# Kernel tuning notes

Measured on AMD Instinct MI355X. Metric: run time of the kernel, lower is better.

The kernel has to match this reference:

```python
import jax, jax.numpy as jnp
import numpy as np

B, IN, H, OUT = 8192, 1024, 1024, 1024


def setup_inputs() -> dict:
    key = jax.random.key(0)
    ks = jax.random.split(key, 17)
    n = jax.random.normal
    return {
        "input": n(ks[0], (B, IN), jnp.float32),
        "hidden_state": n(ks[1], (B, H), jnp.float32),
        "cell_state": n(ks[2], (B, H), jnp.float32),
        "W_f": n(ks[3], (IN, H), jnp.float32),
        "U_f": n(ks[4], (H, H), jnp.float32),
        "b_f": n(ks[5], (H,), jnp.float32),
        "W_i": n(ks[6], (IN, H), jnp.float32),
        "U_i": n(ks[7], (H, H), jnp.float32),
        "b_i": n(ks[8], (H,), jnp.float32),
        "W_c": n(ks[9], (IN, H), jnp.float32),
        "U_c": n(ks[10], (H, H), jnp.float32),
        "b_c": n(ks[11], (H,), jnp.float32),
        "W_o": n(ks[12], (IN, H), jnp.float32),
        "U_o": n(ks[13], (H, H), jnp.float32),
        "b_o": n(ks[14], (H,), jnp.float32),
        "W_h": n(ks[15], (H, OUT), jnp.float32),
        "b_h": n(ks[16], (OUT,), jnp.float32),
    }


def reference(input, hidden_state, cell_state,
              W_f, U_f, b_f, W_i, U_i, b_i,
              W_c, U_c, b_c, W_o, U_o, b_o,
              W_h, b_h):
    # Fuse 8 gate matmuls into two grouped GEMMs via concatenated weights.
    W = jnp.concatenate([W_f, W_i, W_c, W_o], axis=1)  # [IN, 4H]
    U = jnp.concatenate([U_f, U_i, U_c, U_o], axis=1)  # [H, 4H]
    b = jnp.concatenate([b_f, b_i, b_c, b_o], axis=0)  # [4H]
    gates = input @ W + hidden_state @ U + b  # [B, 4H]
    f, i, c, o = jnp.split(gates, 4, axis=1)
    f_gate = jax.nn.sigmoid(f)
    i_gate = jax.nn.sigmoid(i)
    c_tilde = jnp.tanh(c)
    o_gate = jax.nn.sigmoid(o)
    cell_state = f_gate * cell_state + i_gate * c_tilde
    hidden_state = o_gate * jnp.tanh(cell_state)
    logits = hidden_state @ W_h + b_h
    output = jax.nn.log_softmax(logits, axis=1)
    return output, hidden_state, cell_state
```

## Files before the change

### kernel.cpp

```cpp
#include <hip/hip_runtime.h>
#include <hip/hip_bf16.h>
#include <cstdint>


#define B_DIM   8192
#define K1      2048
#define H_DIM   1024

typedef __attribute__((ext_vector_type(8))) _Float16 f16x8;
typedef __attribute__((ext_vector_type(4))) float    f32x4;

__device__ __forceinline__ unsigned short f2h_bits(float x) {
    _Float16 h = (_Float16)x;
    return __builtin_bit_cast(unsigned short, h);
}

__device__ __forceinline__ void gload_lds16(const void* g, void* l) {
    __builtin_amdgcn_global_load_lds(
        (const __attribute__((address_space(1))) void*)g,
        (__attribute__((address_space(3))) void*)l, 16, 0, 0);
}

__device__ __forceinline__ f32x4 mfma16(f16x8 a, f16x8 b, f32x4 c) {
    return __builtin_amdgcn_mfma_f32_16x16x32_f16(a, b, c, 0, 0, 0);
}

__device__ __forceinline__ float vexp2(float x) {
    float r; asm("v_exp_f32 %0, %1" : "=v"(r) : "v"(x)); return r;
}
__device__ __forceinline__ float vlog2(float x) {
    float r; asm("v_log_f32 %0, %1" : "=v"(r) : "v"(x)); return r;
}
__device__ __forceinline__ float vrcp(float x) {
    float r; asm("v_rcp_f32 %0, %1" : "=v"(r) : "v"(x)); return r;
}
__device__ __forceinline__ float fast_sigmoid(float v) {
    return vrcp(1.0f + vexp2(-1.44269504f * v));
}
__device__ __forceinline__ float fast_tanh(float v) {
    return 1.0f - 2.0f * vrcp(1.0f + vexp2(2.88539008f * v));
}

__global__ __launch_bounds__(256) void k_split_x(
    const float* __restrict__ input, const float* __restrict__ hidden,
    unsigned short* __restrict__ xhi) {
    const int64_t n4 = (int64_t)B_DIM * K1 / 4;
    for (int64_t i = (int64_t)blockIdx.x * blockDim.x + threadIdx.x; i < n4;
         i += (int64_t)gridDim.x * blockDim.x) {
        int64_t e = i * 4;
        int row = (int)(e >> 11);
        int col = (int)(e & 2047);
        const float* src = (col < 1024) ? (input + (int64_t)row * 1024 + col)
                                        : (hidden + (int64_t)row * 1024 + (col - 1024));
        float4 v = *(const float4*)src;
        ushort4 hv;
        hv.x = f2h_bits(v.x);
        hv.y = f2h_bits(v.y);
        hv.z = f2h_bits(v.z);
        hv.w = f2h_bits(v.w);
        *(ushort4*)(xhi + e) = hv;
    }
}

__global__ __launch_bounds__(256) void k_trans_all(
    const float* __restrict__ W_f, const float* __restrict__ W_i,
    const float* __restrict__ W_c, const float* __restrict__ W_o,
    const float* __restrict__ U_f, const float* __restrict__ U_i,
    const float* __restrict__ U_c, const float* __restrict__ U_o,
    unsigned short* __restrict__ wuhi) {
    const int z = blockIdx.z;
    const float* src;
    if      (z == 0) src = W_f;
    else if (z == 1) src = W_i;
    else if (z == 2) src = W_c;
    else if (z == 3) src = W_o;
    else if (z == 4) src = U_f;
    else if (z == 5) src = U_i;
    else if (z == 6) src = U_c;
    else             src = U_o;
    const int ng = z & 3, koff = (z >> 2) * 1024;

    __shared__ float t[64][65];
    const int h0 = blockIdx.x * 64;
    const int k0 = blockIdx.y * 64;
    const int tx = threadIdx.x & 63, ty = threadIdx.x >> 6;
    #pragma unroll
    for (int r = ty; r < 64; r += 4)
        t[r][tx] = src[(int64_t)(k0 + r) * 1024 + h0 + tx];
    __syncthreads();
    #pragma unroll
    for (int r = ty; r < 64; r += 4) {
        float v = t[tx][r];
        int np = (h0 + r) * 4 + ng;
        wuhi[(int64_t)np * 2048 + koff + k0 + tx] = f2h_bits(v);
    }
}

__global__ __launch_bounds__(256) void k_trans_wh(
    const float* __restrict__ src, unsigned short* __restrict__ whh) {
    __shared__ float t[64][65];
    const int h0 = blockIdx.x * 64;
    const int k0 = blockIdx.y * 64;
    const int tx = threadIdx.x & 63, ty = threadIdx.x >> 6;
    #pragma unroll
    for (int r = ty; r < 64; r += 4)
        t[r][tx] = src[(int64_t)(k0 + r) * 1024 + h0 + tx];
    __syncthreads();
    #pragma unroll
    for (int r = ty; r < 64; r += 4)
        whh[(int64_t)(h0 + r) * 1024 + k0 + tx] = f2h_bits(t[tx][r]);
}

__global__ __launch_bounds__(256) void k_pack_bias(
    const float* __restrict__ bf_, const float* __restrict__ bi_,
    const float* __restrict__ bc_, const float* __restrict__ bo_,
    float* __restrict__ bias4) {
    int n = blockIdx.x * 256 + threadIdx.x;
    if (n < 4096) {
        int g = n & 3, h = n >> 2;
        const float* p = (g == 0) ? bf_ : (g == 1) ? bi_ : (g == 2) ? bc_ : bo_;
        bias4[n] = p[h];
    }
}

__global__ __launch_bounds__(256, 2) void k_gate_gemm(
    const char* __restrict__ Ah, const char* __restrict__ Bh,
    const float* __restrict__ bias,
    const float* __restrict__ cell,
    float* __restrict__ out0,
    _Float16* __restrict__ hhi) {
    __shared__ char smem[16384];

    const int tid  = threadIdx.x;
    const int lane = tid & 63;
    const int w    = tid >> 6;
    const int wr   = (w >> 1) * 64;
    const int wc   = (w & 1) * 64;
    const int fr   = lane & 15;
    const int q    = lane >> 4;
    const int m0   = blockIdx.y * 128;
    const int n0   = blockIdx.x * 128;

    f32x4 acc[4][4];
    #pragma unroll
    for (int i = 0; i < 4; i++)
        #pragma unroll
        for (int j = 0; j < 4; j++) acc[i][j] = (f32x4){0.f, 0.f, 0.f, 0.f};

    const int srow = tid >> 2;
    const int sg   = (tid & 3) ^ ((tid >> 3) & 3);
    const char* As = Ah + (int64_t)(m0 + srow) * 4096 + sg * 16;
    const char* Bs = Bh + (int64_t)(n0 + srow) * 4096 + sg * 16;

    const unsigned slot = (unsigned)((q ^ ((fr >> 1) & 3)) << 4);

    for (int t = 0; t < 64; ++t) {
        __syncthreads();
        #pragma unroll
        for (int i = 0; i < 2; i++)
            gload_lds16(As + (int64_t)i * 64 * 4096 + t * 64,
                        smem + i * 4096 + tid * 16);
        #pragma unroll
        for (int i = 0; i < 2; i++)
            gload_lds16(Bs + (int64_t)i * 64 * 4096 + t * 64,
                        smem + 8192 + i * 4096 + tid * 16);
        __syncthreads();

        f16x8 ah[4], bh[4];
        #pragma unroll
        for (int mi = 0; mi < 4; mi++)
            ah[mi] = *(const f16x8*)(smem + (wr + mi * 16 + fr) * 64 + slot);
        #pragma unroll
        for (int ni = 0; ni < 4; ni++)
            bh[ni] = *(const f16x8*)(smem + 8192 + (wc + ni * 16 + fr) * 64 + slot);

        #pragma unroll
        for (int ni = 0; ni < 4; ni++)
            #pragma unroll
            for (int mi = 0; mi < 4; mi++)
                acc[mi][ni] = mfma16(ah[mi], bh[ni], acc[mi][ni]);
    }

    const int lb = lane & ~3;
    const int64_t OFF_H = (int64_t)B_DIM * H_DIM;
    const int64_t OFF_C = (int64_t)2 * B_DIM * H_DIM;
    const int g = lane & 3;
    #pragma unroll
    for (int mi = 0; mi < 4; mi++)
        #pragma unroll
        for (int ni = 0; ni < 4; ni++) {
            int col = n0 + wc + ni * 16 + fr;
            int h = col >> 2;
            float bb = bias[col];
            int rowb = m0 + wr + mi * 16 + q * 4;
            #pragma unroll
            for (int j = 0; j < 4; j++) {
                float v = acc[mi][ni][j] + bb;
                float a = (g == 2) ? fast_tanh(v) : fast_sigmoid(v);
                float fg = __shfl(a, lb + 0, 64);
                float ig = __shfl(a, lb + 1, 64);
                float ct = __shfl(a, lb + 2, 64);
                float og = __shfl(a, lb + 3, 64);
                int row = rowb + j;
                int64_t o = (int64_t)row * H_DIM + h;
                float cn = fg * cell[o] + ig * ct;
                float hn = og * fast_tanh(cn);
                if (g == 0) {
                    out0[OFF_C + o] = cn;
                } else if (g == 1) {
                    out0[OFF_H + o] = hn;
                } else if (g == 2) {
                    hhi[o] = (_Float16)hn;
                }
            }
        }
}

__global__ __launch_bounds__(256, 2) void k_gemm128(
    const char* __restrict__ Ah, const char* __restrict__ Bh,
    const float* __restrict__ bias,
    float* __restrict__ out0) {
    __shared__ char smem[16384];

    const int tid  = threadIdx.x;
    const int lane = tid & 63;
    const int w    = tid >> 6;
    const int wr   = (w >> 1) * 64;
    const int wc   = (w & 1) * 64;
    const int m0   = blockIdx.y * 128;
    const int n0   = blockIdx.x * 128;
    const int fr   = lane & 15;
    const int q    = lane >> 4;

    f32x4 acc[4][4];
    #pragma unroll
    for (int i = 0; i < 4; i++)
        #pragma unroll
        for (int j = 0; j < 4; j++) acc[i][j] = (f32x4){0.f, 0.f, 0.f, 0.f};

    const int srow = tid >> 2;
    const int sg   = (tid & 3) ^ ((tid >> 3) & 3);
    const char* Asrc = Ah + (int64_t)(m0 + srow) * 2048 + sg * 16;
    const char* Bsrc = Bh + (int64_t)(n0 + srow) * 2048 + sg * 16;

    const unsigned slot = (unsigned)((q ^ ((fr >> 1) & 3)) << 4);

    for (int t = 0; t < 32; ++t) {
        __syncthreads();
        #pragma unroll
        for (int i = 0; i < 2; i++)
            gload_lds16(Asrc + (int64_t)i * 64 * 2048 + t * 64,
                        smem + i * 4096 + tid * 16);
        #pragma unroll
        for (int i = 0; i < 2; i++)
            gload_lds16(Bsrc + (int64_t)i * 64 * 2048 + t * 64,
                        smem + 8192 + i * 4096 + tid * 16);
        __syncthreads();

        f16x8 ah[4], bh[4];
        #pragma unroll
        for (int mi = 0; mi < 4; mi++)
            ah[mi] = *(const f16x8*)(smem + (wr + mi * 16 + fr) * 64 + slot);
        #pragma unroll
        for (int ni = 0; ni < 4; ni++)
            bh[ni] = *(const f16x8*)(smem + 8192 + (wc + ni * 16 + fr) * 64 + slot);

        #pragma unroll
        for (int ni = 0; ni < 4; ni++)
            #pragma unroll
            for (int mi = 0; mi < 4; mi++)
                acc[mi][ni] = mfma16(ah[mi], bh[ni], acc[mi][ni]);
    }

    #pragma unroll
    for (int mi = 0; mi < 4; mi++)
        #pragma unroll
        for (int ni = 0; ni < 4; ni++) {
            int col = n0 + wc + ni * 16 + fr;
            int rowb = m0 + wr + mi * 16 + q * 4;
            float bb = bias[col];
            #pragma unroll
            for (int j = 0; j < 4; j++)
                out0[(int64_t)(rowb + j) * 1024 + col] = acc[mi][ni][j] + bb;
        }
}

__global__ __launch_bounds__(256) void k_logsoftmax(
    const float* __restrict__ logits, float* __restrict__ out) {
    const int row = blockIdx.x;
    const int t = threadIdx.x;
    const float* x = logits + (int64_t)row * 1024;
    float4 v = *(const float4*)(x + t * 4);

    float m = fmaxf(fmaxf(v.x, v.y), fmaxf(v.z, v.w));
    #pragma unroll
    for (int off = 1; off < 64; off <<= 1) m = fmaxf(m, __shfl_xor(m, off, 64));
    __shared__ float sm[4];
    __shared__ float ssum[4];
    int ln = t & 63, wv = t >> 6;
    if (ln == 0) sm[wv] = m;
    __syncthreads();
    m = fmaxf(fmaxf(sm[0], sm[1]), fmaxf(sm[2], sm[3]));

    const float L2E = 1.44269504f;
    float s = vexp2((v.x - m) * L2E) + vexp2((v.y - m) * L2E)
            + vexp2((v.z - m) * L2E) + vexp2((v.w - m) * L2E);
    #pragma unroll
    for (int off = 1; off < 64; off <<= 1) s += __shfl_xor(s, off, 64);
    if (ln == 0) ssum[wv] = s;
    __syncthreads();
    s = ssum[0] + ssum[1] + ssum[2] + ssum[3];

    float lse = m + vlog2(s) * 0.69314718f;
    float4 o;
    o.x = v.x - lse; o.y = v.y - lse; o.z = v.z - lse; o.w = v.w - lse;
    *(float4*)(out + (int64_t)row * 1024 + t * 4) = o;
}

extern "C" void kernel_launch(void* const* d_in, const int* in_sizes, int n_in,
                              void* d_out, int out_size, void* d_ws, size_t ws_size,
                              hipStream_t stream) {
    const float* input  = (const float*)d_in[0];
    const float* hidden = (const float*)d_in[1];
    const float* cell   = (const float*)d_in[2];
    const float* W_f = (const float*)d_in[3];
    const float* U_f = (const float*)d_in[4];
    const float* b_f = (const float*)d_in[5];
    const float* W_i = (const float*)d_in[6];
    const float* U_i = (const float*)d_in[7];
    const float* b_i = (const float*)d_in[8];
    const float* W_c = (const float*)d_in[9];
    const float* U_c = (const float*)d_in[10];
    const float* b_c = (const float*)d_in[11];
    const float* W_o = (const float*)d_in[12];
    const float* U_o = (const float*)d_in[13];
    const float* b_o = (const float*)d_in[14];
    const float* W_h = (const float*)d_in[15];
    const float* b_h = (const float*)d_in[16];
    float* out = (float*)d_out;

    char* ws = (char*)d_ws;
    unsigned short* xhi  = (unsigned short*)(ws);
    unsigned short* wuhi = (unsigned short*)(ws + 67108864);
    _Float16*       hhi  = (_Float16*)(ws + 83886080);
    unsigned short* whh  = (unsigned short*)(ws + 117440512);
    float*          bias4 = (float*)(ws + 119537664);
    float*          logits = (float*)(ws + 33554432);
    if (ws_size < (size_t)119554048) return;

    k_split_x<<<2048, 256, 0, stream>>>(input, hidden, xhi);
    k_trans_all<<<dim3(16, 16, 8), 256, 0, stream>>>(
        W_f, W_i, W_c, W_o, U_f, U_i, U_c, U_o, wuhi);
    k_trans_wh<<<dim3(16, 16), 256, 0, stream>>>(W_h, whh);
    k_pack_bias<<<16, 256, 0, stream>>>(b_f, b_i, b_c, b_o, bias4);

    k_gate_gemm<<<dim3(32, 64), 256, 0, stream>>>(
        (const char*)xhi, (const char*)wuhi, bias4, cell, out, hhi);

    k_gemm128<<<dim3(8, 64), 256, 0, stream>>>(
        (const char*)hhi, (const char*)whh, b_h, logits);

    k_logsoftmax<<<8192, 256, 0, stream>>>(logits, out);
}
```

Before: 325.3 us.

## Pre-pack gate GEMM operands into MFMA fragment order and load directly to registers

The conversion kernels now write the fp16 activations and gate weights into a panel layout that matches the MFMA 16x16x32 fragment order. The gate GEMM then reads fragments straight from global memory into registers, double-buffered across k-steps, and drops LDS staging and block-wide barriers. The block index is also swizzled to group tiles for better L2 reuse. The cost is that each wave now fetches its own fragments, so there is no LDS sharing between waves, and global-load latency has to be hidden by the two-stage register pipeline.

```diff
diff --git a/kernel.cpp b/kernel.cpp
--- a/kernel.cpp
+++ b/kernel.cpp
@@ -8,6 +8,7 @@
 #define H_DIM   1024
 
 typedef __attribute__((ext_vector_type(8))) _Float16 f16x8;
+typedef __attribute__((ext_vector_type(8))) unsigned short u16x8;
 typedef __attribute__((ext_vector_type(4))) float    f32x4;
 
 __device__ __forceinline__ unsigned short f2h_bits(float x) {
@@ -41,24 +42,31 @@
     return 1.0f - 2.0f * vrcp(1.0f + vexp2(2.88539008f * v));
 }
 
-__global__ __launch_bounds__(256) void k_split_x(
+__device__ __forceinline__ int64_t pan_addr(int r, int k) {
+    int blk = r >> 7, frag = (r >> 4) & 7;
+    int kt = k >> 5, ln = (r & 15) | (((k >> 3) & 3) << 4);
+    return ((int64_t)(blk * 64 + kt) * 8 + frag) * 1024 + ln * 16 + (k & 7) * 2;
+}
+
+__global__ __launch_bounds__(256) void k_pack_x(
     const float* __restrict__ input, const float* __restrict__ hidden,
-    unsigned short* __restrict__ xhi) {
-    const int64_t n4 = (int64_t)B_DIM * K1 / 4;
-    for (int64_t i = (int64_t)blockIdx.x * blockDim.x + threadIdx.x; i < n4;
+    char* __restrict__ Apan) {
+    const int64_t n8 = (int64_t)B_DIM * K1 / 8;
+    for (int64_t i = (int64_t)blockIdx.x * blockDim.x + threadIdx.x; i < n8;
          i += (int64_t)gridDim.x * blockDim.x) {
-        int64_t e = i * 4;
+        int64_t e = i * 8;
         int row = (int)(e >> 11);
         int col = (int)(e & 2047);
         const float* src = (col < 1024) ? (input + (int64_t)row * 1024 + col)
                                         : (hidden + (int64_t)row * 1024 + (col - 1024));
-        float4 v = *(const float4*)src;
-        ushort4 hv;
-        hv.x = f2h_bits(v.x);
-        hv.y = f2h_bits(v.y);
-        hv.z = f2h_bits(v.z);
-        hv.w = f2h_bits(v.w);
-        *(ushort4*)(xhi + e) = hv;
+        float4 v0 = *(const float4*)src;
+        float4 v1 = *(const float4*)(src + 4);
+        u16x8 hv;
+        hv[0] = f2h_bits(v0.x); hv[1] = f2h_bits(v0.y);
+        hv[2] = f2h_bits(v0.z); hv[3] = f2h_bits(v0.w);
+        hv[4] = f2h_bits(v1.x); hv[5] = f2h_bits(v1.y);
+        hv[6] = f2h_bits(v1.z); hv[7] = f2h_bits(v1.w);
+        *(u16x8*)(Apan + pan_addr(row, col)) = hv;
     }
 }
 
@@ -67,7 +75,7 @@
     const float* __restrict__ W_c, const float* __restrict__ W_o,
     const float* __restrict__ U_f, const float* __restrict__ U_i,
     const float* __restrict__ U_c, const float* __restrict__ U_o,
-    unsigned short* __restrict__ wuhi) {
+    char* __restrict__ Bpan) {
     const int z = blockIdx.z;
     const float* src;
     if      (z == 0) src = W_f;
@@ -88,11 +96,14 @@
     for (int r = ty; r < 64; r += 4)
         t[r][tx] = src[(int64_t)(k0 + r) * 1024 + h0 + tx];
     __syncthreads();
-    #pragma unroll
-    for (int r = ty; r < 64; r += 4) {
-        float v = t[tx][r];
-        int np = (h0 + r) * 4 + ng;
-        wuhi[(int64_t)np * 2048 + koff + k0 + tx] = f2h_bits(v);
+    for (int it = threadIdx.x; it < 512; it += 256) {
+        int hl = it >> 3, kg = it & 7;
+        u16x8 hv;
+        #pragma unroll
+        for (int j = 0; j < 8; j++)
+            hv[j] = f2h_bits(t[kg * 8 + j][hl]);
+        int np = (h0 + hl) * 4 + ng;
+        *(u16x8*)(Bpan + pan_addr(np, koff + k0 + kg * 8)) = hv;
     }
 }
 
@@ -124,13 +135,11 @@
 }
 
 __global__ __launch_bounds__(256, 2) void k_gate_gemm(
-    const char* __restrict__ Ah, const char* __restrict__ Bh,
+    const char* __restrict__ Apan, const char* __restrict__ Bpan,
     const float* __restrict__ bias,
     const float* __restrict__ cell,
     float* __restrict__ out0,
     _Float16* __restrict__ hhi) {
-    __shared__ char smem[16384];
-
     const int tid  = threadIdx.x;
     const int lane = tid & 63;
     const int w    = tid >> 6;
@@ -138,8 +147,13 @@
     const int wc   = (w & 1) * 64;
     const int fr   = lane & 15;
     const int q    = lane >> 4;
-    const int m0   = blockIdx.y * 128;
-    const int n0   = blockIdx.x * 128;
+
+    const int lin = blockIdx.y * 32 + blockIdx.x;
+    const int swz = (lin & 7) * 256 + (lin >> 3);
+    const int n_blk = swz & 31;
+    const int m_blk = swz >> 5;
+    const int m0 = m_blk * 128;
+    const int n0 = n_blk * 128;
 
     f32x4 acc[4][4];
     #pragma unroll
@@ -147,39 +161,36 @@
         #pragma unroll
         for (int j = 0; j < 4; j++) acc[i][j] = (f32x4){0.f, 0.f, 0.f, 0.f};
 
-    const int srow = tid >> 2;
-    const int sg   = (tid & 3) ^ ((tid >> 3) & 3);
-    const char* As = Ah + (int64_t)(m0 + srow) * 4096 + sg * 16;
-    const char* Bs = Bh + (int64_t)(n0 + srow) * 4096 + sg * 16;
-
-    const unsigned slot = (unsigned)((q ^ ((fr >> 1) & 3)) << 4);
-
-    for (int t = 0; t < 64; ++t) {
-        __syncthreads();
-        #pragma unroll
-        for (int i = 0; i < 2; i++)
-            gload_lds16(As + (int64_t)i * 64 * 4096 + t * 64,
-                        smem + i * 4096 + tid * 16);
-        #pragma unroll
-        for (int i = 0; i < 2; i++)
-            gload_lds16(Bs + (int64_t)i * 64 * 4096 + t * 64,
-                        smem + 8192 + i * 4096 + tid * 16);
-        __syncthreads();
-
-        f16x8 ah[4], bh[4];
-        #pragma unroll
-        for (int mi = 0; mi < 4; mi++)
-            ah[mi] = *(const f16x8*)(smem + (wr + mi * 16 + fr) * 64 + slot);
-        #pragma unroll
-        for (int ni = 0; ni < 4; ni++)
-            bh[ni] = *(const f16x8*)(smem + 8192 + (wc + ni * 16 + fr) * 64 + slot);
-
-        #pragma unroll
-        for (int ni = 0; ni < 4; ni++)
-            #pragma unroll
-            for (int mi = 0; mi < 4; mi++)
-                acc[mi][ni] = mfma16(ah[mi], bh[ni], acc[mi][ni]);
-    }
+    const char* Ab = Apan + ((int64_t)m_blk * 64 * 8) * 1024
+                          + (wr >> 4) * 1024 + lane * 16;
+    const char* Bb = Bpan + ((int64_t)n_blk * 64 * 8) * 1024
+                          + (wc >> 4) * 1024 + lane * 16;
+
+#define LOADF(AR, BR, KT)                                           \
+    _Pragma("unroll")                                               \
+    for (int mi = 0; mi < 4; mi++)                                  \
+        AR[mi] = *(const f16x8*)(Ab + (int64_t)(KT) * 8192 + mi * 1024); \
+    _Pragma("unroll")                                               \
+    for (int ni = 0; ni < 4; ni++)                                  \
+        BR[ni] = *(const f16x8*)(Bb + (int64_t)(KT) * 8192 + ni * 1024);
+
+#define MFMAF(AR, BR)                                               \
+    _Pragma("unroll")                                               \
+    for (int ni = 0; ni < 4; ni++)                                  \
+        _Pragma("unroll")                                           \
+        for (int mi = 0; mi < 4; mi++)                              \
+            acc[mi][ni] = mfma16(AR[mi], BR[ni], acc[mi][ni]);
+
+    f16x8 a0[4], b0[4], a1[4], b1[4];
+    LOADF(a0, b0, 0);
+    for (int kt = 0; kt < 64; kt += 2) {
+        LOADF(a1, b1, kt + 1);
+        MFMAF(a0, b0);
+        if (kt + 2 < 64) { LOADF(a0, b0, kt + 2); }
+        MFMAF(a1, b1);
+    }
+#undef LOADF
+#undef MFMAF
 
     const int lb = lane & ~3;
     const int64_t OFF_H = (int64_t)B_DIM * H_DIM;
@@ -340,22 +351,22 @@
     float* out = (float*)d_out;
 
     char* ws = (char*)d_ws;
-    unsigned short* xhi  = (unsigned short*)(ws);
-    unsigned short* wuhi = (unsigned short*)(ws + 67108864);
-    _Float16*       hhi  = (_Float16*)(ws + 83886080);
-    unsigned short* whh  = (unsigned short*)(ws + 117440512);
-    float*          bias4 = (float*)(ws + 119537664);
-    float*          logits = (float*)(ws + 33554432);
-    if (ws_size < (size_t)119554048) return;
-
-    k_split_x<<<2048, 256, 0, stream>>>(input, hidden, xhi);
+    char*           Apan = ws;
+    char*           Bpan = ws + 33554432;
+    _Float16*       hhi  = (_Float16*)(ws + 50331648);
+    unsigned short* whh  = (unsigned short*)(ws + 67108864);
+    float*          bias4 = (float*)(ws + 69206016);
+    float*          logits = (float*)(ws);
+    if (ws_size < (size_t)69222400) return;
+
+    k_pack_x<<<2048, 256, 0, stream>>>(input, hidden, Apan);
     k_trans_all<<<dim3(16, 16, 8), 256, 0, stream>>>(
-        W_f, W_i, W_c, W_o, U_f, U_i, U_c, U_o, wuhi);
+        W_f, W_i, W_c, W_o, U_f, U_i, U_c, U_o, Bpan);
     k_trans_wh<<<dim3(16, 16), 256, 0, stream>>>(W_h, whh);
     k_pack_bias<<<16, 256, 0, stream>>>(b_f, b_i, b_c, b_o, bias4);
 
     k_gate_gemm<<<dim3(32, 64), 256, 0, stream>>>(
-        (const char*)xhi, (const char*)wuhi, bias4, cell, out, hhi);
+        Apan, Bpan, bias4, cell, out, hhi);
 
     k_gemm128<<<dim3(8, 64), 256, 0, stream>>>(
         (const char*)hhi, (const char*)whh, b_h, logits);
```

After: 383.7 us. 1.18x slower.
